# Kernel optimization log

Hardware: AMD Instinct MI355X
Metric: run time of the kernel (lower is better)

The kernel has to match this reference:

```python
import jax, jax.numpy as jnp
import numpy as np

B, D, H, L = 65536, 784, 392, 32

def _lin(x, W, b):
    return x @ W.T + b

def setup_inputs() -> dict:
    key = jax.random.key(0)
    ks = jax.random.split(key, 10)
    def w(k, shape):
        fan_in = shape[1]
        return jax.random.normal(k, shape, jnp.float32) * (1.0 / np.sqrt(fan_in))
    return {
        'x': jax.random.uniform(ks[0], (B, D), jnp.float32),
        'eps_z': jax.random.normal(ks[1], (B, L), jnp.float32),
        'eps_y': jax.random.normal(ks[2], (B, D), jnp.float32),
        'W_e1': w(ks[3], (H, D)), 'b_e1': jnp.zeros((H,), jnp.float32),
        'W_emu': w(ks[4], (L, H)), 'b_emu': jnp.zeros((L,), jnp.float32),
        'W_elv': w(ks[5], (L, H)), 'b_elv': jnp.zeros((L,), jnp.float32),
        'W_d1': w(ks[6], (H, L)), 'b_d1': jnp.zeros((H,), jnp.float32),
        'W_dmu': w(ks[7], (D, H)), 'b_dmu': jnp.zeros((D,), jnp.float32),
        'W_dlv': w(ks[8], (D, H)), 'b_dlv': jnp.zeros((D,), jnp.float32),
    }

def reference(x, eps_z, eps_y, W_e1, b_e1, W_emu, b_emu, W_elv, b_elv,
              W_d1, b_d1, W_dmu, b_dmu, W_dlv, b_dlv):
    # encode
    h = jax.nn.relu(_lin(x, W_e1, b_e1))
    mu_z = jax.nn.relu(_lin(h, W_emu, b_emu))
    logvar_z = jax.nn.relu(_lin(h, W_elv, b_elv))
    # reparameterize
    z = mu_z + eps_z * jnp.exp(0.5 * logvar_z)
    # decode
    hd = jax.nn.relu(_lin(z, W_d1, b_d1))
    mu_y = jax.nn.relu(_lin(hd, W_dmu, b_dmu))
    logvar_y = jax.nn.relu(_lin(hd, W_dlv, b_dlv))
    image_res = jax.nn.sigmoid(mu_y + eps_y * jnp.exp(0.5 * logvar_y))
    # NLL: MultivariateNormal(mu, cov=diag(exp(0.5*logvar))).log_prob(x), closed form
    # (original looped per-sample with a Cholesky of a diag matrix; math identical)
    d = mu_y.shape[1]
    var = jnp.exp(0.5 * logvar_y)            # diagonal covariance entries
    quad = jnp.sum((x - mu_y) ** 2 / var, axis=1)
    logdet = jnp.sum(0.5 * logvar_y, axis=1)
    log_prob = -0.5 * (d * jnp.log(2.0 * jnp.pi) + logdet + quad)
    nll = -jnp.mean(log_prob)
    # KL regularisation, faithful to source formula incl. log(1e-8 + exp(logvar))
    kl = jnp.sum(0.5 * jnp.sum(mu_z ** 2 + jnp.exp(logvar_z)
                               - jnp.log(1e-8 + jnp.exp(logvar_z)) - 1.0, axis=1))
    return image_res, nll + kl
```

## Files before the change

kernel.cpp:

```cpp
#include <hip/hip_runtime.h>

#define B_N   65536
#define D_N   784
#define H_N   392
#define L_N   32
#define OUT_IMG ((size_t)B_N * D_N)

typedef unsigned short ushort_t;
typedef __attribute__((ext_vector_type(8))) short short8;
typedef __attribute__((ext_vector_type(4))) float f32x4;

#define N_WE1  358400
#define N_WEZ  26624
#define N_WD1  13312
#define N_WDY  745472
#define N_W16  (N_WE1 + N_WEZ + N_WD1 + N_WDY)
#define N_BIAS 2720
#define WS_BYTES (N_W16*2 + N_BIAS*4)

__device__ __forceinline__ unsigned short f2bf(float f) {
  union { float f; unsigned u; } v; v.f = f;
  unsigned r = v.u + 0x7FFFu + ((v.u >> 16) & 1u);
  return (unsigned short)(r >> 16);
}

__device__ __forceinline__ void gl2lds16(const void* g, void* l) {
  __builtin_amdgcn_global_load_lds(
      (const __attribute__((address_space(1))) unsigned int*)(unsigned long long)g,
      (__attribute__((address_space(3))) unsigned int*)(unsigned int)(unsigned long long)l,
      16, 0, 0);
}

__global__ void vae_prep(const float* __restrict__ We1, const float* __restrict__ Wemu,
                         const float* __restrict__ Welv, const float* __restrict__ Wd1,
                         const float* __restrict__ Wdmu, const float* __restrict__ Wdlv,
                         const float* __restrict__ be1, const float* __restrict__ bemu,
                         const float* __restrict__ belv, const float* __restrict__ bd1,
                         const float* __restrict__ bdmu, const float* __restrict__ bdlv,
                         ushort_t* __restrict__ ws16, float* __restrict__ wsb,
                         float* __restrict__ scalar_out) {
  int idx = blockIdx.x * 256 + threadIdx.x;
  if (idx == 0) *scalar_out = 0.f;
  if (idx < N_W16) {
    float val;
    if (idx < N_WE1) {
      int e = idx; int j = e & 7, lane = (e >> 3) & 63, g = e >> 9;
      int nt = g % 28, kt = g / 28;
      int n = nt * 16 + (lane & 15), k = kt * 32 + ((lane >> 4) << 3) + j;
      val = (n < H_N && k < D_N) ? We1[n * D_N + k] : 0.f;
    } else if (idx < N_WE1 + N_WEZ) {
      int e = idx - N_WE1; int j = e & 7, lane = (e >> 3) & 63, g = e >> 9;
      int kt = g % 13, nt = g / 13;
      int n = nt * 16 + (lane & 15), k = kt * 32 + ((lane >> 4) << 3) + j;
      val = (k < H_N) ? (n < 32 ? Wemu[n * H_N + k] : Welv[(n - 32) * H_N + k]) : 0.f;
    } else if (idx < N_WE1 + N_WEZ + N_WD1) {
      int e = idx - N_WE1 - N_WEZ; int j = e & 7, lane = (e >> 3) & 63, nt = e >> 9;
      int n = nt * 16 + (lane & 15), k = ((lane >> 4) << 3) + j;
      val = (n < H_N) ? Wd1[n * L_N + k] : 0.f;
    } else {
      int e = idx - N_WE1 - N_WEZ - N_WD1; int j = e & 7, lane = (e >> 3) & 63, g = e >> 9;
      int tt = g & 3, nw = (g >> 2) & 3, c = (g >> 4) % 7, kt = g / 112;
      int pair = nw * 14 + 2 * c + (tt >> 1);
      int d = pair * 16 + (lane & 15);
      int k = kt * 32 + ((lane >> 4) << 3) + j;
      val = (d < D_N && k < H_N) ? ((tt & 1) ? Wdlv[d * H_N + k] : Wdmu[d * H_N + k]) : 0.f;
    }
    ws16[idx] = f2bf(val);
  } else {
    int bi = idx - N_W16;
    if (bi < N_BIAS) {
      float val;
      if      (bi < 448)  val = (bi < H_N) ? be1[bi] : 0.f;
      else if (bi < 512)  { int i2 = bi - 448;  val = (i2 < 32) ? bemu[i2] : belv[i2 - 32]; }
      else if (bi < 928)  { int i2 = bi - 512;  val = (i2 < H_N) ? bd1[i2] : 0.f; }
      else if (bi < 1824) { int i2 = bi - 928;  val = (i2 < D_N) ? bdmu[i2] : 0.f; }
      else                { int i2 = bi - 1824; val = (i2 < D_N) ? bdlv[i2] : 0.f; }
      wsb[bi] = val;
    }
  }
}

__global__ __launch_bounds__(512, 2) void vae_main(
    const float* __restrict__ x, const float* __restrict__ eps_z,
    const float* __restrict__ eps_y,
    const ushort_t* __restrict__ ws16, const float* __restrict__ wsb,
    float* __restrict__ out, float* __restrict__ scalar_out) {
  const ushort_t* We1t = ws16;
  const ushort_t* Wezt = ws16 + N_WE1;
  const ushort_t* Wd1t = Wezt + N_WEZ;
  const ushort_t* Wdyt = Wd1t + N_WD1;
  const float* be1p  = wsb;
  const float* bezp  = wsb + 448;
  const float* bd1p  = wsb + 512;
  const float* bdmup = wsb + 928;
  const float* bdlvp = wsb + 1824;

  __shared__ __align__(16) ushort_t hbuf[128 * 424];
  __shared__ __align__(16) ushort_t wslab[28 * 512];
  __shared__ __align__(16) ushort_t xslab[8 * 64 * 8];
  __shared__ __align__(16) ushort_t zbuf[128 * 40];
  __shared__ float red[8];

  const int tid  = threadIdx.x;
  const int w    = tid >> 6;
  const int lane = tid & 63;
  const int quad = lane >> 4;
  const int l16  = lane & 15;
  const int mw   = w >> 2, nw = w & 3;
  const int rb   = blockIdx.x * 128;

  float kl_acc = 0.f, q_acc = 0.f, ld_acc = 0.f;

  f32x4 acc1[4][7];
  {
    f32x4 z4 = {0.f, 0.f, 0.f, 0.f};
#pragma unroll
    for (int i = 0; i < 4; ++i)
#pragma unroll
      for (int t = 0; t < 7; ++t) acc1[i][t] = z4;
  }
  const int sr = tid >> 2, sq = tid & 3;
  for (int kt = 0; kt < 25; ++kt) {
    __syncthreads();
#pragma unroll
    for (int i = 0; i < 4; ++i) {
      int g = i * 512 + tid;
      if (g < 1792) gl2lds16((const char*)We1t + kt * 28672 + g * 16, (char*)wslab + g * 16);
    }
    {
      int4 P;
      if (kt == 24 && sq >= 2) { P.x = 0; P.y = 0; P.z = 0; P.w = 0; }
      else {
        const float4* px = (const float4*)(x + (size_t)(rb + sr) * D_N + kt * 32 + sq * 8);
        float4 v0 = px[0], v1 = px[1];
        P.x = f2bf(v0.x) | ((unsigned)f2bf(v0.y) << 16);
        P.y = f2bf(v0.z) | ((unsigned)f2bf(v0.w) << 16);
        P.z = f2bf(v1.x) | ((unsigned)f2bf(v1.y) << 16);
        P.w = f2bf(v1.z) | ((unsigned)f2bf(v1.w) << 16);
      }
      ((int4*)xslab)[(sr >> 4) * 64 + (sq << 4) + (sr & 15)] = P;
    }
    __syncthreads();
    short8 afr[4];
#pragma unroll
    for (int i = 0; i < 4; ++i)
      afr[i] = *(const short8*)(xslab + ((mw * 4 + i) * 64 + lane) * 8);
#pragma unroll
    for (int t = 0; t < 7; ++t) {
      short8 bfr = *(const short8*)(wslab + ((nw * 7 + t) * 64 + lane) * 8);
#pragma unroll
      for (int i = 0; i < 4; ++i)
        acc1[i][t] = __builtin_amdgcn_mfma_f32_16x16x32_bf16(afr[i], bfr, acc1[i][t], 0, 0, 0);
    }
  }
#pragma unroll
  for (int t = 0; t < 7; ++t) {
    int ntg = nw * 7 + t;
    if (ntg < 26) {
      int n = ntg * 16 + l16;
      float bb = be1p[n];
#pragma unroll
      for (int i = 0; i < 4; ++i)
#pragma unroll
        for (int r = 0; r < 4; ++r) {
          int m = mw * 64 + i * 16 + quad * 4 + r;
          hbuf[m * 424 + n] = f2bf(fmaxf(acc1[i][t][r] + bb, 0.f));
        }
    }
  }
  __syncthreads();

  f32x4 acc2[4];
  {
    f32x4 z4 = {0.f, 0.f, 0.f, 0.f};
#pragma unroll
    for (int nt = 0; nt < 4; ++nt) acc2[nt] = z4;
  }
  for (int kt = 0; kt < 13; ++kt) {
    short8 a = *(const short8*)(hbuf + (16 * w + l16) * 424 + kt * 32 + quad * 8);
#pragma unroll
    for (int nt = 0; nt < 4; ++nt) {
      short8 b = *(const short8*)(Wezt + ((nt * 13 + kt) * 64 + lane) * 8);
      acc2[nt] = __builtin_amdgcn_mfma_f32_16x16x32_bf16(a, b, acc2[nt], 0, 0, 0);
    }
  }
#pragma unroll
  for (int s = 0; s < 2; ++s) {
    float bmu = bezp[s * 16 + l16];
    float blv = bezp[32 + s * 16 + l16];
#pragma unroll
    for (int r = 0; r < 4; ++r) {
      float mu = fmaxf(acc2[s][r] + bmu, 0.f);
      float lv = fmaxf(acc2[s + 2][r] + blv, 0.f);
      int m = 16 * w + quad * 4 + r;
      int gm = rb + m;
      int l = s * 16 + l16;
      float e = expf(lv);
      kl_acc += 0.5f * (mu * mu + e - logf(1e-8f + e) - 1.f);
      float zz = mu + eps_z[gm * 32 + l] * expf(0.5f * lv);
      zbuf[m * 40 + l] = f2bf(zz);
    }
  }
  __syncthreads();

  {
    short8 az = *(const short8*)(zbuf + (16 * w + l16) * 40 + quad * 8);
    for (int nt = 0; nt < 26; ++nt) {
      short8 b = *(const short8*)(Wd1t + (nt * 64 + lane) * 8);
      f32x4 a4 = {0.f, 0.f, 0.f, 0.f};
      a4 = __builtin_amdgcn_mfma_f32_16x16x32_bf16(az, b, a4, 0, 0, 0);
      int n = nt * 16 + l16;
      float bb = bd1p[n];
#pragma unroll
      for (int r = 0; r < 4; ++r) {
        int m = 16 * w + quad * 4 + r;
        hbuf[m * 424 + n] = f2bf(fmaxf(a4[r] + bb, 0.f));
      }
    }
  }

  for (int c = 0; c < 7; ++c) {
    f32x4 acc5[4][4];
    {
      f32x4 z4 = {0.f, 0.f, 0.f, 0.f};
#pragma unroll
      for (int i = 0; i < 4; ++i)
#pragma unroll
        for (int tt = 0; tt < 4; ++tt) acc5[i][tt] = z4;
    }
    for (int kt = 0; kt < 13; ++kt) {
      __syncthreads();
#pragma unroll
      for (int i = 0; i < 2; ++i) {
        int g = i * 512 + tid;
        gl2lds16((const char*)Wdyt + (kt * 7 + c) * 16384 + g * 16, (char*)wslab + g * 16);
      }
      __syncthreads();
      short8 a[4];
#pragma unroll
      for (int i = 0; i < 4; ++i)
        a[i] = *(const short8*)(hbuf + (mw * 64 + i * 16 + l16) * 424 + kt * 32 + quad * 8);
#pragma unroll
      for (int tt = 0; tt < 4; ++tt) {
        short8 b = *(const short8*)(wslab + ((nw * 4 + tt) * 64 + lane) * 8);
#pragma unroll
        for (int i = 0; i < 4; ++i)
          acc5[i][tt] = __builtin_amdgcn_mfma_f32_16x16x32_bf16(a[i], b, acc5[i][tt], 0, 0, 0);
      }
    }
#pragma unroll
    for (int s = 0; s < 2; ++s) {
      int d = (nw * 14 + 2 * c + s) * 16 + l16;
      if (d < D_N) {
        float bmu = bdmup[d], blv = bdlvp[d];
#pragma unroll
        for (int i = 0; i < 4; ++i) {
#pragma unroll
          for (int r = 0; r < 4; ++r) {
            int m = mw * 64 + i * 16 + quad * 4 + r;
            size_t gi = (size_t)(rb + m) * D_N + d;
            float mu = fmaxf(acc5[i][2 * s][r] + bmu, 0.f);
            float lv = fmaxf(acc5[i][2 * s + 1][r] + blv, 0.f);
            float sd = expf(0.5f * lv);
            float tval = mu + eps_y[gi] * sd;
            out[gi] = 1.f / (1.f + expf(-tval));
            float dq = x[gi] - mu;
            q_acc  += dq * dq / sd;
            ld_acc += 0.5f * lv;
          }
        }
      }
    }
  }

  float v = (0.5f / (float)B_N) * (ld_acc + q_acc) + kl_acc;
#pragma unroll
  for (int off = 32; off; off >>= 1) v += __shfl_down(v, off, 64);
  if (lane == 0) red[w] = v;
  __syncthreads();
  if (tid == 0) {
    float tot = 0.f;
#pragma unroll
    for (int i = 0; i < 8; ++i) tot += red[i];
    if (blockIdx.x == 0) tot += 720.447808f;
    atomicAdd(scalar_out, tot);
  }
}

extern "C" void kernel_launch(void* const* d_in, const int* in_sizes, int n_in,
                              void* d_out, int out_size, void* d_ws, size_t ws_size,
                              hipStream_t stream) {
  const float* x     = (const float*)d_in[0];
  const float* eps_z = (const float*)d_in[1];
  const float* eps_y = (const float*)d_in[2];
  const float* We1   = (const float*)d_in[3];
  const float* be1   = (const float*)d_in[4];
  const float* Wemu  = (const float*)d_in[5];
  const float* bemu  = (const float*)d_in[6];
  const float* Welv  = (const float*)d_in[7];
  const float* belv  = (const float*)d_in[8];
  const float* Wd1   = (const float*)d_in[9];
  const float* bd1   = (const float*)d_in[10];
  const float* Wdmu  = (const float*)d_in[11];
  const float* bdmu  = (const float*)d_in[12];
  const float* Wdlv  = (const float*)d_in[13];
  const float* bdlv  = (const float*)d_in[14];

  float* out = (float*)d_out;
  float* scalar_out = out + OUT_IMG;

  ushort_t* ws16 = (ushort_t*)d_ws;
  float* wsb = (float*)((char*)d_ws + (size_t)N_W16 * 2);

  int prep_total = N_W16 + N_BIAS;
  int prep_blocks = (prep_total + 255) / 256;
  vae_prep<<<prep_blocks, 256, 0, stream>>>(We1, Wemu, Welv, Wd1, Wdmu, Wdlv,
                                            be1, bemu, belv, bd1, bdmu, bdlv,
                                            ws16, wsb, scalar_out);

  vae_main<<<B_N / 128, 512, 0, stream>>>(x, eps_z, eps_y, ws16, wsb, out, scalar_out);
}
```

Before: 874.7 us.

## Load weights and x fragments directly from global, dropping LDS staging and barriers

The first and last GEMMs now read the pre-swizzled weight fragments and x fragments straight from global memory into registers instead of staging them through LDS with global_load_lds and two barriers per k-step. This removes the wslab and xslab buffers and most __syncthreads, and trims the hbuf row stride from 424 to 420. It also adds s_setprio around the MFMA blocks, unrolls the k-loops by two, moves one barrier, and swaps expf, logf and division for the fast intrinsics. The cost is redundant global/L2 traffic, since every wave fetches its own weight fragments, and slightly lower precision in the transcendental functions.

```diff
diff --git a/kernel.cpp b/kernel.cpp
--- a/kernel.cpp
+++ b/kernel.cpp
@@ -5,6 +5,8 @@
 #define H_N   392
 #define L_N   32
 #define OUT_IMG ((size_t)B_N * D_N)
+
+#define HSTR  420
 
 typedef unsigned short ushort_t;
 typedef __attribute__((ext_vector_type(8))) short short8;
@@ -22,13 +24,6 @@
   union { float f; unsigned u; } v; v.f = f;
   unsigned r = v.u + 0x7FFFu + ((v.u >> 16) & 1u);
   return (unsigned short)(r >> 16);
-}
-
-__device__ __forceinline__ void gl2lds16(const void* g, void* l) {
-  __builtin_amdgcn_global_load_lds(
-      (const __attribute__((address_space(1))) unsigned int*)(unsigned long long)g,
-      (__attribute__((address_space(3))) unsigned int*)(unsigned int)(unsigned long long)l,
-      16, 0, 0);
 }
 
 __global__ void vae_prep(const float* __restrict__ We1, const float* __restrict__ Wemu,
@@ -95,9 +90,7 @@
   const float* bdmup = wsb + 928;
   const float* bdlvp = wsb + 1824;
 
-  __shared__ __align__(16) ushort_t hbuf[128 * 424];
-  __shared__ __align__(16) ushort_t wslab[28 * 512];
-  __shared__ __align__(16) ushort_t xslab[8 * 64 * 8];
+  __shared__ __align__(16) ushort_t hbuf[128 * HSTR];
   __shared__ __align__(16) ushort_t zbuf[128 * 40];
   __shared__ float red[8];
 
@@ -119,35 +112,55 @@
 #pragma unroll
       for (int t = 0; t < 7; ++t) acc1[i][t] = z4;
   }
-  const int sr = tid >> 2, sq = tid & 3;
-  for (int kt = 0; kt < 25; ++kt) {
-    __syncthreads();
+  const float* xp[4];
+#pragma unroll
+  for (int i = 0; i < 4; ++i)
+    xp[i] = x + (size_t)(rb + mw * 64 + i * 16 + l16) * D_N + quad * 8;
+
+#pragma unroll 2
+  for (int kt = 0; kt < 24; ++kt) {
+    short8 afr[4];
 #pragma unroll
     for (int i = 0; i < 4; ++i) {
-      int g = i * 512 + tid;
-      if (g < 1792) gl2lds16((const char*)We1t + kt * 28672 + g * 16, (char*)wslab + g * 16);
-    }
-    {
-      int4 P;
-      if (kt == 24 && sq >= 2) { P.x = 0; P.y = 0; P.z = 0; P.w = 0; }
-      else {
-        const float4* px = (const float4*)(x + (size_t)(rb + sr) * D_N + kt * 32 + sq * 8);
+      const float4* px = (const float4*)(xp[i] + kt * 32);
+      float4 v0 = px[0], v1 = px[1];
+      union { int4 p; short8 s; } u;
+      u.p.x = f2bf(v0.x) | ((unsigned)f2bf(v0.y) << 16);
+      u.p.y = f2bf(v0.z) | ((unsigned)f2bf(v0.w) << 16);
+      u.p.z = f2bf(v1.x) | ((unsigned)f2bf(v1.y) << 16);
+      u.p.w = f2bf(v1.z) | ((unsigned)f2bf(v1.w) << 16);
+      afr[i] = u.s;
+    }
+    __builtin_amdgcn_s_setprio(1);
+#pragma unroll
+    for (int t = 0; t < 7; ++t) {
+      short8 bfr = *(const short8*)(We1t + ((kt * 28 + nw * 7 + t) * 64 + lane) * 8);
+#pragma unroll
+      for (int i = 0; i < 4; ++i)
+        acc1[i][t] = __builtin_amdgcn_mfma_f32_16x16x32_bf16(afr[i], bfr, acc1[i][t], 0, 0, 0);
+    }
+    __builtin_amdgcn_s_setprio(0);
+  }
+  {
+    short8 afr[4];
+#pragma unroll
+    for (int i = 0; i < 4; ++i) {
+      union { int4 p; short8 s; } u;
+      if (quad < 2) {
+        const float4* px = (const float4*)(xp[i] + 24 * 32);
         float4 v0 = px[0], v1 = px[1];
-        P.x = f2bf(v0.x) | ((unsigned)f2bf(v0.y) << 16);
-        P.y = f2bf(v0.z) | ((unsigned)f2bf(v0.w) << 16);
-        P.z = f2bf(v1.x) | ((unsigned)f2bf(v1.y) << 16);
-        P.w = f2bf(v1.z) | ((unsigned)f2bf(v1.w) << 16);
+        u.p.x = f2bf(v0.x) | ((unsigned)f2bf(v0.y) << 16);
+        u.p.y = f2bf(v0.z) | ((unsigned)f2bf(v0.w) << 16);
+        u.p.z = f2bf(v1.x) | ((unsigned)f2bf(v1.y) << 16);
+        u.p.w = f2bf(v1.z) | ((unsigned)f2bf(v1.w) << 16);
+      } else {
+        u.p.x = 0; u.p.y = 0; u.p.z = 0; u.p.w = 0;
       }
-      ((int4*)xslab)[(sr >> 4) * 64 + (sq << 4) + (sr & 15)] = P;
-    }
-    __syncthreads();
-    short8 afr[4];
-#pragma unroll
-    for (int i = 0; i < 4; ++i)
-      afr[i] = *(const short8*)(xslab + ((mw * 4 + i) * 64 + lane) * 8);
+      afr[i] = u.s;
+    }
 #pragma unroll
     for (int t = 0; t < 7; ++t) {
-      short8 bfr = *(const short8*)(wslab + ((nw * 7 + t) * 64 + lane) * 8);
+      short8 bfr = *(const short8*)(We1t + ((24 * 28 + nw * 7 + t) * 64 + lane) * 8);
 #pragma unroll
       for (int i = 0; i < 4; ++i)
         acc1[i][t] = __builtin_amdgcn_mfma_f32_16x16x32_bf16(afr[i], bfr, acc1[i][t], 0, 0, 0);
@@ -164,7 +177,7 @@
 #pragma unroll
         for (int r = 0; r < 4; ++r) {
           int m = mw * 64 + i * 16 + quad * 4 + r;
-          hbuf[m * 424 + n] = f2bf(fmaxf(acc1[i][t][r] + bb, 0.f));
+          hbuf[m * HSTR + n] = f2bf(fmaxf(acc1[i][t][r] + bb, 0.f));
         }
     }
   }
@@ -177,7 +190,7 @@
     for (int nt = 0; nt < 4; ++nt) acc2[nt] = z4;
   }
   for (int kt = 0; kt < 13; ++kt) {
-    short8 a = *(const short8*)(hbuf + (16 * w + l16) * 424 + kt * 32 + quad * 8);
+    short8 a = *(const short8*)(hbuf + (16 * w + l16) * HSTR + kt * 32 + quad * 8);
 #pragma unroll
     for (int nt = 0; nt < 4; ++nt) {
       short8 b = *(const short8*)(Wezt + ((nt * 13 + kt) * 64 + lane) * 8);
@@ -195,13 +208,12 @@
       int m = 16 * w + quad * 4 + r;
       int gm = rb + m;
       int l = s * 16 + l16;
-      float e = expf(lv);
-      kl_acc += 0.5f * (mu * mu + e - logf(1e-8f + e) - 1.f);
-      float zz = mu + eps_z[gm * 32 + l] * expf(0.5f * lv);
+      float e = __expf(lv);
+      kl_acc += 0.5f * (mu * mu + e - __logf(1e-8f + e) - 1.f);
+      float zz = mu + eps_z[gm * 32 + l] * __expf(0.5f * lv);
       zbuf[m * 40 + l] = f2bf(zz);
     }
   }
-  __syncthreads();
 
   {
     short8 az = *(const short8*)(zbuf + (16 * w + l16) * 40 + quad * 8);
@@ -214,10 +226,11 @@
 #pragma unroll
       for (int r = 0; r < 4; ++r) {
         int m = 16 * w + quad * 4 + r;
-        hbuf[m * 424 + n] = f2bf(fmaxf(a4[r] + bb, 0.f));
+        hbuf[m * HSTR + n] = f2bf(fmaxf(a4[r] + bb, 0.f));
       }
     }
   }
+  __syncthreads();
 
   for (int c = 0; c < 7; ++c) {
     f32x4 acc5[4][4];
@@ -228,25 +241,22 @@
 #pragma unroll
         for (int tt = 0; tt < 4; ++tt) acc5[i][tt] = z4;
     }
+#pragma unroll 2
     for (int kt = 0; kt < 13; ++kt) {
-      __syncthreads();
-#pragma unroll
-      for (int i = 0; i < 2; ++i) {
-        int g = i * 512 + tid;
-        gl2lds16((const char*)Wdyt + (kt * 7 + c) * 16384 + g * 16, (char*)wslab + g * 16);
-      }
-      __syncthreads();
-      short8 a[4];
-#pragma unroll
-      for (int i = 0; i < 4; ++i)
-        a[i] = *(const short8*)(hbuf + (mw * 64 + i * 16 + l16) * 424 + kt * 32 + quad * 8);
-#pragma unroll
-      for (int tt = 0; tt < 4; ++tt) {
-        short8 b = *(const short8*)(wslab + ((nw * 4 + tt) * 64 + lane) * 8);
+      short8 a[4], b[4];
+#pragma unroll
+      for (int i = 0; i < 4; ++i)
+        a[i] = *(const short8*)(hbuf + (mw * 64 + i * 16 + l16) * HSTR + kt * 32 + quad * 8);
+#pragma unroll
+      for (int tt = 0; tt < 4; ++tt)
+        b[tt] = *(const short8*)(Wdyt + ((kt * 112 + c * 16 + nw * 4 + tt) * 64 + lane) * 8);
+      __builtin_amdgcn_s_setprio(1);
+#pragma unroll
+      for (int tt = 0; tt < 4; ++tt)
 #pragma unroll
         for (int i = 0; i < 4; ++i)
-          acc5[i][tt] = __builtin_amdgcn_mfma_f32_16x16x32_bf16(a[i], b, acc5[i][tt], 0, 0, 0);
-      }
+          acc5[i][tt] = __builtin_amdgcn_mfma_f32_16x16x32_bf16(a[i], b[tt], acc5[i][tt], 0, 0, 0);
+      __builtin_amdgcn_s_setprio(0);
     }
 #pragma unroll
     for (int s = 0; s < 2; ++s) {
@@ -261,11 +271,11 @@
             size_t gi = (size_t)(rb + m) * D_N + d;
             float mu = fmaxf(acc5[i][2 * s][r] + bmu, 0.f);
             float lv = fmaxf(acc5[i][2 * s + 1][r] + blv, 0.f);
-            float sd = expf(0.5f * lv);
+            float sd = __expf(0.5f * lv);
             float tval = mu + eps_y[gi] * sd;
-            out[gi] = 1.f / (1.f + expf(-tval));
+            out[gi] = __builtin_amdgcn_rcpf(1.f + __expf(-tval));
             float dq = x[gi] - mu;
-            q_acc  += dq * dq / sd;
+            q_acc  += dq * dq * __builtin_amdgcn_rcpf(sd);
             ld_acc += 0.5f * lv;
           }
         }
```

New measurement: 1.264 ms. 1.44x slower.
